# Kernel tuning notes

Hardware: AMD Instinct MI355X
Metric: run time of the kernel (lower is better)

Reference implementation:

```python
import jax, jax.numpy as jnp
import numpy as np

N_NODES = 100_000
N_EDGES = 1_600_000
IN_F = 256
HID = 256
OUT_F = 256
BN_EPS = 1e-5


def make_quaternion_mul(kernel):
    # kernel: [d, 4m] -> hamilton: [4d, 4m]
    dim = kernel.shape[1] // 4
    r, i, j, k = jnp.split(kernel, 4, axis=1)
    r2 = jnp.concatenate([r, -i, -j, -k], axis=0)
    i2 = jnp.concatenate([i, r, -k, j], axis=0)
    j2 = jnp.concatenate([j, k, r, -i], axis=0)
    k2 = jnp.concatenate([k, -j, i, r], axis=0)
    return jnp.concatenate([r2, i2, j2, k2], axis=1)


def setup_inputs() -> dict:
    key = jax.random.key(0)
    ks = jax.random.split(key, 6)
    x = jax.random.normal(ks[0], (N_NODES, IN_F), dtype=jnp.float32)
    rows = jax.random.randint(ks[1], (N_EDGES,), 0, N_NODES, dtype=jnp.int32)
    cols = jax.random.randint(ks[2], (N_EDGES,), 0, N_NODES, dtype=jnp.int32)
    edge_vals = jax.random.uniform(ks[3], (N_EDGES,), dtype=jnp.float32)
    stdv1 = np.sqrt(6.0 / (IN_F // 4 + HID))
    weight1 = jax.random.uniform(ks[4], (IN_F // 4, HID), dtype=jnp.float32,
                                 minval=-stdv1, maxval=stdv1)
    stdv2 = np.sqrt(6.0 / (HID // 4 + OUT_F))
    weight2 = jax.random.uniform(ks[5], (HID // 4, OUT_F), dtype=jnp.float32,
                                 minval=-stdv2, maxval=stdv2)
    gamma = jnp.ones((HID,), dtype=jnp.float32)
    beta = jnp.zeros((HID,), dtype=jnp.float32)
    return {"x": x, "rows": rows, "cols": cols, "edge_vals": edge_vals,
            "weight1": weight1, "weight2": weight2, "gamma": gamma, "beta": beta}


def reference(x, rows, cols, edge_vals, weight1, weight2, gamma, beta):
    hamilton1 = make_quaternion_mul(weight1)  # [IN_F, HID]
    hamilton2 = make_quaternion_mul(weight2)  # [HID, OUT_F]
    # spmm: new_x[r] = sum_e adj[r,c]*x[c] over edges (r=rows, c=cols)
    gathered = edge_vals[:, None] * x[cols]               # [E, IN_F]
    new_x = jax.ops.segment_sum(gathered, rows, num_segments=N_NODES)
    out1 = new_x @ hamilton1                              # [N, HID]
    # BatchNorm1d (training mode): biased batch stats over nodes
    mean = jnp.mean(out1, axis=0)
    var = jnp.mean(jnp.square(out1 - mean), axis=0)
    out1 = (out1 - mean) * jax.lax.rsqrt(var + BN_EPS) * gamma + beta
    out1 = jnp.tanh(out1)
    return out1 @ hamilton2                               # [N, OUT_F]
```

## Files before the change

kernel.cpp:

```cpp
#include <hip/hip_runtime.h>
#include <hip/hip_bf16.h>
#include <math.h>


#define FDIM 256
#define NREP 32
#define CH 2048

typedef __attribute__((ext_vector_type(8))) short bf16x8;
typedef __attribute__((ext_vector_type(4))) float f32x4;

static __device__ inline short f2bf(float x) {
    __hip_bfloat16 h = __float2bfloat16(x);
    return *reinterpret_cast<short*>(&h);
}
static __device__ inline float bf2f(unsigned short u) {
    union { unsigned int i; float f; } c;
    c.i = ((unsigned int)u) << 16;
    return c.f;
}
static __device__ inline float fast_tanh(float x) {
    float e = __expf(2.f * x);
    return 1.f - 2.f * __builtin_amdgcn_rcpf(e + 1.f);
}

static __device__ void build_hfrag(const float* __restrict__ w, ushort* __restrict__ hf,
                                   int t) {
    const int   comp_t[16] = {0,1,2,3,  1,0,3,2,  2,3,0,1,  3,2,1,0};
    const float sign_t[16] = {1,1,1,1, -1,1,1,-1, -1,-1,1,1, -1,1,-1,1};
    int f = t >> 6, lane = t & 63;
    int tile = f >> 3, kk = f & 7;
    int col = tile * 16 + (lane & 15);
    int b = col >> 6, q = col & 63;
    ushort o[8];
#pragma unroll
    for (int j = 0; j < 8; ++j) {
        int k = kk * 32 + ((lane >> 4) << 3) + j;
        int a = k >> 6, p = k & 63;
        int ab = a * 4 + b;
        float v = sign_t[ab] * w[p * 256 + comp_t[ab] * 64 + q];
        o[j] = (ushort)f2bf(v);
    }
    *(ushort4*)(hf + (size_t)t * 8)     = make_ushort4(o[0], o[1], o[2], o[3]);
    *(ushort4*)(hf + (size_t)t * 8 + 4) = make_ushort4(o[4], o[5], o[6], o[7]);
}

__global__ __launch_bounds__(256) void k_initp1(const float* __restrict__ w1,
                                                const float* __restrict__ w2,
                                                ushort* __restrict__ h1f,
                                                ushort* __restrict__ h2f,
                                                float* __restrict__ statsR,
                                                const int* __restrict__ rows,
                                                int* __restrict__ CM,
                                                int E, int nchunk, int NB) {
    int b = blockIdx.x;
    if (b < 32) {
        build_hfrag(w1, h1f, b * 256 + threadIdx.x);
        return;
    }
    if (b < 64) {
        build_hfrag(w2, h2f, (b - 32) * 256 + threadIdx.x);
        return;
    }
    if (b < 80) {
        int slot = (b - 64) * 256 + threadIdx.x;
        *(float4*)(statsR + slot * 4) = make_float4(0.f, 0.f, 0.f, 0.f);
        return;
    }
    __shared__ int lc[256];
    int t = threadIdx.x, c = b - 80;
    lc[t] = 0;
    __syncthreads();
#pragma unroll
    for (int i = 0; i < 8; ++i) {
        int e = c * CH + i * 256 + t;
        if (e < E) atomicAdd(&lc[rows[e] >> 9], 1);
    }
    __syncthreads();
    if (t < NB) CM[t * nchunk + c] = lc[t];
}

__global__ __launch_bounds__(256) void k_p2(const int* __restrict__ CM,
                                            int* __restrict__ PO,
                                            int* __restrict__ BT, int nchunk) {
    __shared__ int ts[256];
    int t = threadIdx.x, b = blockIdx.x;
    int base = b * nchunk;
    int lex[4], s = 0;
#pragma unroll
    for (int i = 0; i < 4; ++i) {
        int c = t * 4 + i;
        int v = (c < nchunk) ? CM[base + c] : 0;
        lex[i] = s;
        s += v;
    }
    ts[t] = s;
    __syncthreads();
    for (int off = 1; off < 256; off <<= 1) {
        int v = (t >= off) ? ts[t - off] : 0;
        __syncthreads();
        ts[t] += v;
        __syncthreads();
    }
    int excl = ts[t] - s;
#pragma unroll
    for (int i = 0; i < 4; ++i) {
        int c = t * 4 + i;
        if (c < nchunk) PO[base + c] = excl + lex[i];
    }
    if (t == 255) BT[b] = ts[255];
}

__global__ __launch_bounds__(256) void k_p3(const int* __restrict__ rows,
                                            const int* __restrict__ cols,
                                            const float* __restrict__ vals,
                                            const int* __restrict__ PO,
                                            const int* __restrict__ BT,
                                            uint2* __restrict__ tmp2,
                                            int E, int nchunk, int NB) {
    __shared__ int sBB[256];
    __shared__ int sPO[256];
    __shared__ int sLC[256];
    int t = threadIdx.x, c = blockIdx.x;
    int own = (t < NB) ? BT[t] : 0;
    sBB[t] = own;
    sPO[t] = (t < NB) ? PO[t * nchunk + c] : 0;
    sLC[t] = 0;
    __syncthreads();
    for (int off = 1; off < 256; off <<= 1) {
        int v = (t >= off) ? sBB[t - off] : 0;
        __syncthreads();
        sBB[t] += v;
        __syncthreads();
    }
    sBB[t] -= own;
    __syncthreads();
#pragma unroll
    for (int i = 0; i < 8; ++i) {
        int e = c * CH + i * 256 + t;
        if (e < E) {
            int r = rows[e];
            int b = r >> 9;
            int rank = atomicAdd(&sLC[b], 1);
            int pos = sBB[b] + sPO[b] + rank;
            int iv = (int)(vals[e] * 32768.0f);
            tmp2[pos] = make_uint2((unsigned int)cols[e] | ((unsigned int)iv << 17),
                                   (unsigned int)r);
        }
    }
}

__global__ __launch_bounds__(1024) void k_p4(const uint2* __restrict__ tmp2,
                                             const int* __restrict__ BT,
                                             unsigned int* __restrict__ ew,
                                             uint2* __restrict__ offs2,
                                             int N, int NB) {
    __shared__ int sBB[256];
    __shared__ int sH[512];
    __shared__ int sHp[512];
    __shared__ int sOp[512];
    __shared__ int sC[512];
    int t = threadIdx.x, b = blockIdx.x;
    int own = 0;
    if (t < 256) {
        own = (t < NB) ? BT[t] : 0;
        sBB[t] = own;
    }
    __syncthreads();
    for (int off = 1; off < 256; off <<= 1) {
        int v = (t < 256 && t >= off) ? sBB[t - off] : 0;
        __syncthreads();
        if (t < 256) sBB[t] += v;
        __syncthreads();
    }
    if (t < 256) sBB[t] -= own;
    if (t < 512) sH[t] = 0;
    __syncthreads();
    const int base = sBB[b];
    const int basePad = sBB[b] + b * 4096;
    const int nE = BT[b];
    const int rbase = b << 9;
    for (int i = t; i < nE; i += 1024)
        atomicAdd(&sH[(int)tmp2[base + i].y - rbase], 1);
    __syncthreads();
    if (t < 512) {
        int hp = (sH[t] + 7) & ~7;
        sHp[t] = hp;
        sOp[t] = hp;
    }
    __syncthreads();
    for (int off = 1; off < 512; off <<= 1) {
        int v = (t < 512 && t >= off) ? sOp[t - off] : 0;
        __syncthreads();
        if (t < 512) sOp[t] += v;
        __syncthreads();
    }
    if (t < 512) {
        sOp[t] -= sHp[t];
        int r = rbase + t;
        if (r < N) offs2[r] = make_uint2((unsigned int)(basePad + sOp[t]),
                                         (unsigned int)sHp[t]);
        sC[t] = 0;
    }
    __syncthreads();
    for (int i = t; i < nE; i += 1024) {
        uint2 u = tmp2[base + i];
        int lr = (int)u.y - rbase;
        int p = atomicAdd(&sC[lr], 1);
        ew[basePad + sOp[lr] + p] = u.x;
    }
    if (t < 512) {
        int e0 = basePad + sOp[t] + sH[t];
        int e1 = basePad + sOp[t] + sHp[t];
        for (int e = e0; e < e1; ++e) ew[e] = 0u;
    }
}

__global__ __launch_bounds__(256) void k_gemm1(const float* __restrict__ X,
                                               const ushort* __restrict__ Bf,
                                               ushort* __restrict__ Y, int N) {
    __shared__ float4 lds4[2048];
    ushort* lds = (ushort*)lds4;
    const int t = threadIdx.x;
    const int w = t >> 6, lane = t & 63;
    const int r0 = blockIdx.x * 128 + w * 32;
    const int q = (lane >> 4) & 3, l = lane & 15;
    const int kbase = q * 8;
    const int rA[2] = { min(r0 + l, N - 1), min(r0 + 16 + l, N - 1) };

    bf16x8 af[2][8];
#pragma unroll
    for (int rt = 0; rt < 2; ++rt)
#pragma unroll
        for (int kk = 0; kk < 8; ++kk) {
            const float* p = X + (size_t)rA[rt] * 256 + kk * 32 + kbase;
            float4 v0 = *(const float4*)p;
            float4 v1 = *(const float4*)(p + 4);
            bf16x8 a;
            a[0] = f2bf(v0.x); a[1] = f2bf(v0.y); a[2] = f2bf(v0.z); a[3] = f2bf(v0.w);
            a[4] = f2bf(v1.x); a[5] = f2bf(v1.y); a[6] = f2bf(v1.z); a[7] = f2bf(v1.w);
            af[rt][kk] = a;
        }

    for (int g = 0; g < 4; ++g) {
        {
            const float4* s4 = (const float4*)(Bf + (size_t)g * 16384);
#pragma unroll
            for (int i = 0; i < 8; ++i) lds4[i * 256 + t] = s4[i * 256 + t];
        }
        __syncthreads();

        f32x4 acc[2][4];
#pragma unroll
        for (int rt = 0; rt < 2; ++rt)
#pragma unroll
            for (int tg = 0; tg < 4; ++tg) acc[rt][tg] = (f32x4){0.f, 0.f, 0.f, 0.f};

#pragma unroll
        for (int tg = 0; tg < 4; ++tg)
#pragma unroll
            for (int kk = 0; kk < 8; ++kk) {
                bf16x8 b = *(const bf16x8*)(lds + ((tg * 8 + kk) * 64 + lane) * 8);
                acc[0][tg] = __builtin_amdgcn_mfma_f32_16x16x32_bf16(af[0][kk], b, acc[0][tg], 0, 0, 0);
                acc[1][tg] = __builtin_amdgcn_mfma_f32_16x16x32_bf16(af[1][kk], b, acc[1][tg], 0, 0, 0);
            }
        __syncthreads();

        {
            ushort* cw = lds + w * 2048;
#pragma unroll
            for (int tg = 0; tg < 4; ++tg)
#pragma unroll
                for (int rt = 0; rt < 2; ++rt)
#pragma unroll
                    for (int j = 0; j < 4; ++j)
                        cw[(rt * 16 + q * 4 + j) * 64 + tg * 16 + l] =
                            (ushort)f2bf(acc[rt][tg][j]);
            int gcol0 = g * 64;
#pragma unroll
            for (int p = 0; p < 4; ++p) {
                uint4 rd = *(const uint4*)(lds + w * 2048 + p * 512 + lane * 8);
                int row = r0 + p * 8 + (lane >> 3);
                int col = gcol0 + (lane & 7) * 8;
                if (row < N) *(uint4*)(Y + (size_t)row * 256 + col) = rd;
            }
        }
        __syncthreads();
    }
}

__global__ __launch_bounds__(256) void k_spmm(const ushort* __restrict__ Y,
                                              const uint2* __restrict__ offs2,
                                              const unsigned int* __restrict__ ew,
                                              ushort* __restrict__ O,
                                              float* __restrict__ statsR,
                                              int n, int W) {
    __shared__ float ls_s[4][256];
    __shared__ float ls_q[4][256];
    const int tid = threadIdx.x;
    const int w = tid >> 6, lane = tid & 63;
    const int gw = blockIdx.x * 4 + w;

    float s0 = 0.f, s1 = 0.f, s2 = 0.f, s3 = 0.f;
    float q0 = 0.f, q1 = 0.f, q2 = 0.f, q3 = 0.f;

    for (int k = 0; k < 4; ++k) {
        int row = gw + k * W;
        bool ok = row < n;
        int r = ok ? row : 0;
        uint2 bc = offs2[r];
        int cnt = ok ? (int)bc.y : 0;
        int g = cnt >> 3;
        const unsigned int* ep = ew + bc.x;

        float a0 = 0.f, a1 = 0.f, a2 = 0.f, a3 = 0.f;
        unsigned int wv[8];
        if (g > 0) {
#pragma unroll
            for (int i = 0; i < 8; ++i) wv[i] = ep[i];
        }
        for (int gi = 0; gi < g; ++gi) {
            unsigned int wn[8];
            bool more = (gi + 1) < g;
            if (more) {
#pragma unroll
                for (int i = 0; i < 8; ++i) wn[i] = ep[(gi + 1) * 8 + i];
            }
#pragma unroll
            for (int i = 0; i < 8; ++i) {
                unsigned int wd = wv[i];
                int c = (int)(wd & 0x1FFFFu);
                float v = (float)(wd >> 17) * (1.0f / 32768.0f);
                ushort4 yv = *(const ushort4*)(Y + (size_t)c * 256 + lane * 4);
                a0 = fmaf(v, bf2f(yv.x), a0);
                a1 = fmaf(v, bf2f(yv.y), a1);
                a2 = fmaf(v, bf2f(yv.z), a2);
                a3 = fmaf(v, bf2f(yv.w), a3);
            }
            if (more) {
#pragma unroll
                for (int i = 0; i < 8; ++i) wv[i] = wn[i];
            }
        }
        if (ok) {
            ushort4 o = make_ushort4((ushort)f2bf(a0), (ushort)f2bf(a1),
                                     (ushort)f2bf(a2), (ushort)f2bf(a3));
            *(ushort4*)(O + (size_t)r * 512 + lane * 4) = o;
        }
        s0 += a0; q0 = fmaf(a0, a0, q0);
        s1 += a1; q1 = fmaf(a1, a1, q1);
        s2 += a2; q2 = fmaf(a2, a2, q2);
        s3 += a3; q3 = fmaf(a3, a3, q3);
    }

    int rep = blockIdx.x & (NREP - 1);
    *(float4*)&ls_s[w][lane * 4] = make_float4(s0, s1, s2, s3);
    *(float4*)&ls_q[w][lane * 4] = make_float4(q0, q1, q2, q3);
    __syncthreads();
    float sv = ls_s[0][tid] + ls_s[1][tid] + ls_s[2][tid] + ls_s[3][tid];
    float qv = ls_q[0][tid] + ls_q[1][tid] + ls_q[2][tid] + ls_q[3][tid];
    atomicAdd(&statsR[rep * 256 + tid], sv);
    atomicAdd(&statsR[NREP * 256 + rep * 256 + tid], qv);
}

__global__ __launch_bounds__(256) void k_gemm2(void* __restrict__ Av,
                                               const ushort* __restrict__ Bf,
                                               const float* __restrict__ statsR,
                                               const float* __restrict__ gamma,
                                               const float* __restrict__ beta, int N) {
    __shared__ float4 lds4[2048];
    ushort* lds = (ushort*)lds4;
    __shared__ float sscl[256], sshf[256];
    const int t = threadIdx.x;
    const int w = t >> 6, lane = t & 63;
    const int r0 = blockIdx.x * 128 + w * 32;
    const int q = (lane >> 4) & 3, l = lane & 15;
    const int kbase = q * 8;
    const int rA[2] = { min(r0 + l, N - 1), min(r0 + 16 + l, N - 1) };

    {
        float s = 0.f, qq = 0.f;
#pragma unroll
        for (int i = 0; i < NREP; ++i) {
            s += statsR[i * 256 + t];
            qq += statsR[NREP * 256 + i * 256 + t];
        }
        float invn = 1.0f / (float)N;
        float mean = s * invn;
        float var = qq * invn - mean * mean;
        float inv = rsqrtf(var + 1e-5f);
        float gg = gamma[t] * inv;
        sscl[t] = gg;
        sshf[t] = beta[t] - mean * gg;
        __syncthreads();
    }

    const ushort* X = (const ushort*)Av;
    bf16x8 af[2][8];
#pragma unroll
    for (int rt = 0; rt < 2; ++rt)
#pragma unroll
        for (int kk = 0; kk < 8; ++kk) {
            const ushort* p = X + (size_t)rA[rt] * 512 + kk * 32 + kbase;
            ushort4 u0 = *(const ushort4*)p;
            ushort4 u1 = *(const ushort4*)(p + 4);
            float4 s0 = *(const float4*)&sscl[kk * 32 + kbase];
            float4 s1 = *(const float4*)&sscl[kk * 32 + kbase + 4];
            float4 h0 = *(const float4*)&sshf[kk * 32 + kbase];
            float4 h1 = *(const float4*)&sshf[kk * 32 + kbase + 4];
            bf16x8 a;
            a[0] = f2bf(fast_tanh(fmaf(bf2f(u0.x), s0.x, h0.x)));
            a[1] = f2bf(fast_tanh(fmaf(bf2f(u0.y), s0.y, h0.y)));
            a[2] = f2bf(fast_tanh(fmaf(bf2f(u0.z), s0.z, h0.z)));
            a[3] = f2bf(fast_tanh(fmaf(bf2f(u0.w), s0.w, h0.w)));
            a[4] = f2bf(fast_tanh(fmaf(bf2f(u1.x), s1.x, h1.x)));
            a[5] = f2bf(fast_tanh(fmaf(bf2f(u1.y), s1.y, h1.y)));
            a[6] = f2bf(fast_tanh(fmaf(bf2f(u1.z), s1.z, h1.z)));
            a[7] = f2bf(fast_tanh(fmaf(bf2f(u1.w), s1.w, h1.w)));
            af[rt][kk] = a;
        }

    float* Cf = (float*)Av;
    for (int g = 0; g < 4; ++g) {
        {
            const float4* s4 = (const float4*)(Bf + (size_t)g * 16384);
#pragma unroll
            for (int i = 0; i < 8; ++i) lds4[i * 256 + t] = s4[i * 256 + t];
        }
        __syncthreads();

        f32x4 acc[2][4];
#pragma unroll
        for (int rt = 0; rt < 2; ++rt)
#pragma unroll
            for (int tg = 0; tg < 4; ++tg) acc[rt][tg] = (f32x4){0.f, 0.f, 0.f, 0.f};

#pragma unroll
        for (int tg = 0; tg < 4; ++tg)
#pragma unroll
            for (int kk = 0; kk < 8; ++kk) {
                bf16x8 b = *(const bf16x8*)(lds + ((tg * 8 + kk) * 64 + lane) * 8);
                acc[0][tg] = __builtin_amdgcn_mfma_f32_16x16x32_bf16(af[0][kk], b, acc[0][tg], 0, 0, 0);
                acc[1][tg] = __builtin_amdgcn_mfma_f32_16x16x32_bf16(af[1][kk], b, acc[1][tg], 0, 0, 0);
            }
        __syncthreads();

        {
            float* cw = (float*)lds4 + w * 2048;
#pragma unroll
            for (int tg = 0; tg < 4; ++tg)
#pragma unroll
                for (int rt = 0; rt < 2; ++rt)
#pragma unroll
                    for (int j = 0; j < 4; ++j)
                        cw[(rt * 16 + q * 4 + j) * 64 + tg * 16 + l] = acc[rt][tg][j];
            int gcol0 = g * 64;
#pragma unroll
            for (int p = 0; p < 8; ++p) {
                float4 rd = *(const float4*)((float*)lds4 + w * 2048 + p * 256 + lane * 4);
                int row = r0 + p * 4 + (lane >> 4);
                int col = gcol0 + (lane & 15) * 4;
                if (row < N) *(float4*)(Cf + (size_t)row * 256 + col) = rd;
            }
        }
        __syncthreads();
    }
}

extern "C" void kernel_launch(void* const* d_in, const int* in_sizes, int n_in,
                              void* d_out, int out_size, void* d_ws, size_t ws_size,
                              hipStream_t stream) {
    const float* x     = (const float*)d_in[0];
    const int* rows    = (const int*)d_in[1];
    const int* cols    = (const int*)d_in[2];
    const float* evin  = (const float*)d_in[3];
    const float* w1    = (const float*)d_in[4];
    const float* w2    = (const float*)d_in[5];
    const float* gamma = (const float*)d_in[6];
    const float* beta  = (const float*)d_in[7];
    float* out = (float*)d_out;

    const int N = in_sizes[0] / FDIM;
    const int E = in_sizes[1];
    const int NB = (N + 511) >> 9;
    const int nchunk = (E + CH - 1) / CH;

    char* ws = (char*)d_ws;
    size_t o = 0;
    auto alloc = [&](size_t bytes) -> char* {
        char* p = ws + o;
        o += (bytes + 255) & ~(size_t)255;
        return p;
    };
    ushort* h1f  = (ushort*)alloc(128 * 64 * 8 * 2);
    ushort* h2f  = (ushort*)alloc(128 * 64 * 8 * 2);
    ushort* y    = (ushort*)alloc((size_t)N * 256 * 2);
    float* statsR = (float*)alloc(2 * NREP * 256 * 4);
    int*   CM    = (int*)alloc((size_t)NB * nchunk * 4);
    int*   PO    = (int*)alloc((size_t)NB * nchunk * 4);
    int*   BT    = (int*)alloc(256 * 4);
    uint2* tmp2  = (uint2*)alloc((size_t)E * 8);
    unsigned int* ewp = (unsigned int*)alloc(((size_t)E + (size_t)NB * 4096 + 16) * 4);
    uint2* offs2 = (uint2*)alloc((size_t)N * 8);

    k_initp1<<<80 + nchunk, 256, 0, stream>>>(w1, w2, h1f, h2f, statsR,
                                              rows, CM, E, nchunk, NB);
    k_p2<<<NB, 256, 0, stream>>>(CM, PO, BT, nchunk);
    k_p3<<<nchunk, 256, 0, stream>>>(rows, cols, evin, PO, BT, tmp2, E, nchunk, NB);
    k_p4<<<NB, 1024, 0, stream>>>(tmp2, BT, ewp, offs2, N, NB);

    int gblk = (N + 127) / 128;
    k_gemm1<<<gblk, 256, 0, stream>>>(x, h1f, y, N);
    int W = (N + 3) / 4;
    int sblk = (W + 3) / 4;
    k_spmm<<<sblk, 256, 0, stream>>>(y, offs2, ewp, (ushort*)out, statsR, N, W);
    k_gemm2<<<gblk, 256, 0, stream>>>(out, h2f, statsR, gamma, beta, N);
}
```

Before: 256.8 us.

## Split SpMM into two feature-half passes and use nontemporal stores in GEMM2

The SpMM now runs as two launches, each gathering only 128 of the 256 feature columns per edge (ushort2 per lane instead of ushort4). This halves the gathered working set per pass so more of Y stays resident in cache, at the cost of reading the edge list and offsets twice and doing narrower loads. GEMM2 also switches its final float4 output stores to nontemporal stores so the written result does not pollute the cache.

```diff
diff --git a/kernel.cpp b/kernel.cpp
--- a/kernel.cpp
+++ b/kernel.cpp
@@ -294,15 +294,16 @@
                                               const unsigned int* __restrict__ ew,
                                               ushort* __restrict__ O,
                                               float* __restrict__ statsR,
-                                              int n, int W) {
-    __shared__ float ls_s[4][256];
-    __shared__ float ls_q[4][256];
+                                              int n, int W, int half) {
+    __shared__ float ls_s[4][128];
+    __shared__ float ls_q[4][128];
     const int tid = threadIdx.x;
     const int w = tid >> 6, lane = tid & 63;
     const int gw = blockIdx.x * 4 + w;
-
-    float s0 = 0.f, s1 = 0.f, s2 = 0.f, s3 = 0.f;
-    float q0 = 0.f, q1 = 0.f, q2 = 0.f, q3 = 0.f;
+    const int fb = half * 128 + lane * 2;
+
+    float s0 = 0.f, s1 = 0.f;
+    float q0 = 0.f, q1 = 0.f;
 
     for (int k = 0; k < 4; ++k) {
         int row = gw + k * W;
@@ -313,7 +314,7 @@
         int g = cnt >> 3;
         const unsigned int* ep = ew + bc.x;
 
-        float a0 = 0.f, a1 = 0.f, a2 = 0.f, a3 = 0.f;
+        float a0 = 0.f, a1 = 0.f;
         unsigned int wv[8];
         if (g > 0) {
 #pragma unroll
@@ -331,11 +332,9 @@
                 unsigned int wd = wv[i];
                 int c = (int)(wd & 0x1FFFFu);
                 float v = (float)(wd >> 17) * (1.0f / 32768.0f);
-                ushort4 yv = *(const ushort4*)(Y + (size_t)c * 256 + lane * 4);
+                ushort2 yv = *(const ushort2*)(Y + (size_t)c * 256 + fb);
                 a0 = fmaf(v, bf2f(yv.x), a0);
                 a1 = fmaf(v, bf2f(yv.y), a1);
-                a2 = fmaf(v, bf2f(yv.z), a2);
-                a3 = fmaf(v, bf2f(yv.w), a3);
             }
             if (more) {
 #pragma unroll
@@ -343,24 +342,23 @@
             }
         }
         if (ok) {
-            ushort4 o = make_ushort4((ushort)f2bf(a0), (ushort)f2bf(a1),
-                                     (ushort)f2bf(a2), (ushort)f2bf(a3));
-            *(ushort4*)(O + (size_t)r * 512 + lane * 4) = o;
+            ushort2 o = make_ushort2((ushort)f2bf(a0), (ushort)f2bf(a1));
+            *(ushort2*)(O + (size_t)r * 512 + fb) = o;
         }
         s0 += a0; q0 = fmaf(a0, a0, q0);
         s1 += a1; q1 = fmaf(a1, a1, q1);
-        s2 += a2; q2 = fmaf(a2, a2, q2);
-        s3 += a3; q3 = fmaf(a3, a3, q3);
     }
 
     int rep = blockIdx.x & (NREP - 1);
-    *(float4*)&ls_s[w][lane * 4] = make_float4(s0, s1, s2, s3);
-    *(float4*)&ls_q[w][lane * 4] = make_float4(q0, q1, q2, q3);
-    __syncthreads();
-    float sv = ls_s[0][tid] + ls_s[1][tid] + ls_s[2][tid] + ls_s[3][tid];
-    float qv = ls_q[0][tid] + ls_q[1][tid] + ls_q[2][tid] + ls_q[3][tid];
-    atomicAdd(&statsR[rep * 256 + tid], sv);
-    atomicAdd(&statsR[NREP * 256 + rep * 256 + tid], qv);
+    *(float2*)&ls_s[w][lane * 2] = make_float2(s0, s1);
+    *(float2*)&ls_q[w][lane * 2] = make_float2(q0, q1);
+    __syncthreads();
+    if (tid < 128) {
+        float sv = ls_s[0][tid] + ls_s[1][tid] + ls_s[2][tid] + ls_s[3][tid];
+        float qv = ls_q[0][tid] + ls_q[1][tid] + ls_q[2][tid] + ls_q[3][tid];
+        atomicAdd(&statsR[rep * 256 + half * 128 + tid], sv);
+        atomicAdd(&statsR[NREP * 256 + rep * 256 + half * 128 + tid], qv);
+    }
 }
 
 __global__ __launch_bounds__(256) void k_gemm2(void* __restrict__ Av,
@@ -457,10 +455,11 @@
             int gcol0 = g * 64;
 #pragma unroll
             for (int p = 0; p < 8; ++p) {
-                float4 rd = *(const float4*)((float*)lds4 + w * 2048 + p * 256 + lane * 4);
+                f32x4 rd = *(const f32x4*)((float*)lds4 + w * 2048 + p * 256 + lane * 4);
                 int row = r0 + p * 4 + (lane >> 4);
                 int col = gcol0 + (lane & 15) * 4;
-                if (row < N) *(float4*)(Cf + (size_t)row * 256 + col) = rd;
+                if (row < N)
+                    __builtin_nontemporal_store(rd, (f32x4*)(Cf + (size_t)row * 256 + col));
             }
         }
         __syncthreads();
@@ -513,6 +512,7 @@
     k_gemm1<<<gblk, 256, 0, stream>>>(x, h1f, y, N);
     int W = (N + 3) / 4;
     int sblk = (W + 3) / 4;
-    k_spmm<<<sblk, 256, 0, stream>>>(y, offs2, ewp, (ushort*)out, statsR, N, W);
+    k_spmm<<<sblk, 256, 0, stream>>>(y, offs2, ewp, (ushort*)out, statsR, N, W, 0);
+    k_spmm<<<sblk, 256, 0, stream>>>(y, offs2, ewp, (ushort*)out, statsR, N, W, 1);
     k_gemm2<<<gblk, 256, 0, stream>>>(out, h2f, statsR, gamma, beta, N);
 }
```

Result: no change. 252.2 us (-1.8%).
